# Performance work log

Measured on AMD Instinct MI355X. Metric: run time of the kernel, lower is better.

## Reference

```python
import jax, jax.numpy as jnp
import numpy as np

SEQ_DIM = 256
PAIR_DIM = 128
N_HEADS = 8
HIDDEN = 32
B, L = 4, 512


def layer_norm(x, gamma, beta, eps=1e-5):
    mu = jnp.mean(x, axis=-1, keepdims=True)
    var = jnp.var(x, axis=-1, keepdims=True)
    return (x - mu) * jax.lax.rsqrt(var + eps) * gamma + beta


def setup_inputs() -> dict:
    key = jax.random.key(0)
    ks = jax.random.split(key, 12)
    d = N_HEADS * HIDDEN
    s = 0.02
    return {
        "seq": jax.random.normal(ks[0], (B, L, SEQ_DIM), jnp.float32),
        "pair": jax.random.normal(ks[1], (B, L, L, PAIR_DIM), jnp.float32),
        "ln_seq_g": jnp.ones((SEQ_DIM,), jnp.float32),
        "ln_seq_b": jnp.zeros((SEQ_DIM,), jnp.float32),
        "ln_pair_g": jnp.ones((PAIR_DIM,), jnp.float32),
        "ln_pair_b": jnp.zeros((PAIR_DIM,), jnp.float32),
        "W_b": jax.random.normal(ks[2], (PAIR_DIM, N_HEADS), jnp.float32) * s,
        "W_q": jax.random.normal(ks[3], (SEQ_DIM, d), jnp.float32) * s,
        "W_k": jax.random.normal(ks[4], (SEQ_DIM, d), jnp.float32) * s,
        "W_v": jax.random.normal(ks[5], (SEQ_DIM, d), jnp.float32) * s,
        "W_g": jax.random.normal(ks[6], (SEQ_DIM, d), jnp.float32) * s,
        "b_g": jnp.zeros((d,), jnp.float32),
        "W_o": jax.random.normal(ks[7], (d, SEQ_DIM), jnp.float32) * s,
        "b_o": jnp.zeros((SEQ_DIM,), jnp.float32),
    }


def reference(seq, pair, ln_seq_g, ln_seq_b, ln_pair_g, ln_pair_b,
              W_b, W_q, W_k, W_v, W_g, b_g, W_o, b_o):
    b, l, _ = seq.shape
    factor = 1.0 / np.sqrt(HIDDEN).astype(np.float32)
    s = layer_norm(seq, ln_seq_g, ln_seq_b)
    p = layer_norm(pair, ln_pair_g, ln_pair_b)
    Q = (s @ W_q).reshape(b, l, N_HEADS, HIDDEN)
    K = (s @ W_k).reshape(b, l, N_HEADS, HIDDEN)
    V = (s @ W_v).reshape(b, l, N_HEADS, HIDDEN)
    # pair bias: [b, i, j, n] -> [b, n, i, j]
    bias = jnp.einsum('bijp,pn->bnij', p, W_b)
    att = jnp.einsum('binh,bjnh->bnij', Q, K) * factor + bias
    att = jax.nn.softmax(att, axis=-1)
    gate = jax.nn.sigmoid(s @ W_g + b_g).reshape(b, l, N_HEADS, HIDDEN)
    out = jnp.einsum('bnij,bjnh->binh', att, V) * gate
    out = out.reshape(b, l, N_HEADS * HIDDEN)
    return out @ W_o + b_o
```

## Files before the change

### kernel.cpp

```cpp
#include <hip/hip_runtime.h>
#include <math.h>

#define OFF_Q    0
#define OFF_K    (524288)
#define OFF_V    (524288*2)
#define OFF_G    (524288*3)
#define OFF_PRE  (524288*4)
#define OFF_BIAS (524288*5)

template <int CTRL>
__device__ __forceinline__ float dpp_mov(float x) {
  return __int_as_float(__builtin_amdgcn_update_dpp(0, __float_as_int(x), CTRL, 0xF, 0xF, true));
}
template <int CTRL>
__device__ __forceinline__ float dpp_add(float x) { return x + dpp_mov<CTRL>(x); }
__device__ __forceinline__ float red16(float v) {
  v = dpp_add<0xB1>(v);
  v = dpp_add<0x4E>(v);
  v = dpp_add<0x141>(v);
  v = dpp_add<0x140>(v);
  return v;
}

#define SEL8(a, f, out) do { \
  float _s0 = ((f)&1) ? a[1] : a[0]; \
  float _s1 = ((f)&1) ? a[3] : a[2]; \
  float _s2 = ((f)&1) ? a[5] : a[4]; \
  float _s3 = ((f)&1) ? a[7] : a[6]; \
  float _t0 = ((f)&2) ? _s1 : _s0; \
  float _t1 = ((f)&2) ? _s3 : _s2; \
  out = ((f)&4) ? _t1 : _t0; \
} while(0)

__device__ __forceinline__ float4 sel8_f4(const float4* a, int f) {
  float4 s0 = (f&1) ? a[1] : a[0];
  float4 s1 = (f&1) ? a[3] : a[2];
  float4 s2 = (f&1) ? a[5] : a[4];
  float4 s3 = (f&1) ? a[7] : a[6];
  float4 t0 = (f&2) ? s1 : s0;
  float4 t1 = (f&2) ? s3 : s2;
  return (f&4) ? t1 : t0;
}

__device__ __forceinline__ float dot4(float4 a, float4 b, float acc) {
  acc = fmaf(a.x, b.x, acc); acc = fmaf(a.y, b.y, acc);
  acc = fmaf(a.z, b.z, acc); return fmaf(a.w, b.w, acc);
}

template <int CTRL>
__device__ __forceinline__ void merge_dpp(float& m, float& l, float4* acc) {
  float m2 = dpp_mov<CTRL>(m);
  float l2 = dpp_mov<CTRL>(l);
  float M = fmaxf(m, m2);
  float ea = __expf(m - M), eb = __expf(m2 - M);
  l = l*ea + l2*eb;
#pragma unroll
  for (int x = 0; x < 8; ++x) {
    acc[x].x = acc[x].x*ea + dpp_mov<CTRL>(acc[x].x)*eb;
    acc[x].y = acc[x].y*ea + dpp_mov<CTRL>(acc[x].y)*eb;
    acc[x].z = acc[x].z*ea + dpp_mov<CTRL>(acc[x].z)*eb;
    acc[x].w = acc[x].w*ea + dpp_mov<CTRL>(acc[x].w)*eb;
  }
  m = M;
}

__global__ __launch_bounds__(256, 3) void k_mega(
    const float* __restrict__ seq, const float* __restrict__ lsg, const float* __restrict__ lsb,
    const float* __restrict__ lpg, const float* __restrict__ lpb, const float* __restrict__ Wb,
    const float* __restrict__ Wq, const float* __restrict__ Wk, const float* __restrict__ Wv,
    const float* __restrict__ Wg, const float* __restrict__ bg, const float* __restrict__ pair,
    float* __restrict__ Qw, float* __restrict__ Kw, float* __restrict__ Vw, float* __restrict__ Gw,
    float* __restrict__ biasw) {
  __shared__ __align__(16) float As[256*36];
  int t = threadIdx.x;
  int blk = blockIdx.x;

  if (blk >= 512) {
    int kb = blk - 512;
    int m0 = (kb >> 3) * 32;
    int y = kb & 7;
    {
      int r = t >> 3, c0 = t & 7;
      const float* srow = seq + (size_t)(m0 + r) * 256;
      float4 v[8];
      float s = 0.f, sq = 0.f;
#pragma unroll
      for (int qq = 0; qq < 8; ++qq) {
        v[qq] = *(const float4*)(srow + 4*(c0 + 8*qq));
        s += v[qq].x + v[qq].y + v[qq].z + v[qq].w;
        sq = fmaf(v[qq].x, v[qq].x, sq); sq = fmaf(v[qq].y, v[qq].y, sq);
        sq = fmaf(v[qq].z, v[qq].z, sq); sq = fmaf(v[qq].w, v[qq].w, sq);
      }
#pragma unroll
      for (int mm = 1; mm < 8; mm <<= 1) { s += __shfl_xor(s, mm); sq += __shfl_xor(sq, mm); }
      float mu = s * (1.f/256.f);
      float var = sq * (1.f/256.f) - mu*mu;
      float rstd = rsqrtf(var + 1e-5f);
#pragma unroll
      for (int qq = 0; qq < 8; ++qq) {
        int c4 = c0 + 8*qq;
        float4 g  = *(const float4*)(lsg + 4*c4);
        float4 bb = *(const float4*)(lsb + 4*c4);
        float* dp = As + 4*c4*36 + r;
        dp[0]   = (v[qq].x - mu)*rstd*g.x + bb.x;
        dp[36]  = (v[qq].y - mu)*rstd*g.y + bb.y;
        dp[72]  = (v[qq].z - mu)*rstd*g.z + bb.z;
        dp[108] = (v[qq].w - mu)*rstd*g.w + bb.w;
      }
    }
    __syncthreads();
    const float* Wm = (y < 2) ? Wq : (y < 4) ? Wk : (y < 6) ? Wv : Wg;
    int cb = (y & 1) * 128;
    int rg = t >> 5, cg2 = t & 31;
    const float* bp = Wm + cb + 4*cg2;
    const float* ap = As + 4*rg;
    float4 a0 = {0,0,0,0}, a1 = {0,0,0,0}, a2 = {0,0,0,0}, a3 = {0,0,0,0};
#pragma unroll 4
    for (int p = 0; p < 256; ++p) {
      float4 a  = *(const float4*)(ap + p*36);
      float4 bv = *(const float4*)(bp + p*256);
      a0.x = fmaf(a.x, bv.x, a0.x); a0.y = fmaf(a.x, bv.y, a0.y);
      a0.z = fmaf(a.x, bv.z, a0.z); a0.w = fmaf(a.x, bv.w, a0.w);
      a1.x = fmaf(a.y, bv.x, a1.x); a1.y = fmaf(a.y, bv.y, a1.y);
      a1.z = fmaf(a.y, bv.z, a1.z); a1.w = fmaf(a.y, bv.w, a1.w);
      a2.x = fmaf(a.z, bv.x, a2.x); a2.y = fmaf(a.z, bv.y, a2.y);
      a2.z = fmaf(a.z, bv.z, a2.z); a2.w = fmaf(a.z, bv.w, a2.w);
      a3.x = fmaf(a.w, bv.x, a3.x); a3.y = fmaf(a.w, bv.y, a3.y);
      a3.z = fmaf(a.w, bv.z, a3.z); a3.w = fmaf(a.w, bv.w, a3.w);
    }
    int mat = y >> 1;
    int col = cb + 4*cg2;
    float* outp = (mat == 0) ? Qw : (mat == 1) ? Kw : (mat == 2) ? Vw : Gw;
    if (mat == 0) {
      const float qs = 0.17677669529663687f;
      a0.x*=qs; a0.y*=qs; a0.z*=qs; a0.w*=qs;
      a1.x*=qs; a1.y*=qs; a1.z*=qs; a1.w*=qs;
      a2.x*=qs; a2.y*=qs; a2.z*=qs; a2.w*=qs;
      a3.x*=qs; a3.y*=qs; a3.z*=qs; a3.w*=qs;
    }
    if (mat == 3) {
      float4 g4 = *(const float4*)(bg + col);
      a0.x = 1.f/(1.f+__expf(-(a0.x+g4.x))); a0.y = 1.f/(1.f+__expf(-(a0.y+g4.y)));
      a0.z = 1.f/(1.f+__expf(-(a0.z+g4.z))); a0.w = 1.f/(1.f+__expf(-(a0.w+g4.w)));
      a1.x = 1.f/(1.f+__expf(-(a1.x+g4.x))); a1.y = 1.f/(1.f+__expf(-(a1.y+g4.y)));
      a1.z = 1.f/(1.f+__expf(-(a1.z+g4.z))); a1.w = 1.f/(1.f+__expf(-(a1.w+g4.w)));
      a2.x = 1.f/(1.f+__expf(-(a2.x+g4.x))); a2.y = 1.f/(1.f+__expf(-(a2.y+g4.y)));
      a2.z = 1.f/(1.f+__expf(-(a2.z+g4.z))); a2.w = 1.f/(1.f+__expf(-(a2.w+g4.w)));
      a3.x = 1.f/(1.f+__expf(-(a3.x+g4.x))); a3.y = 1.f/(1.f+__expf(-(a3.y+g4.y)));
      a3.z = 1.f/(1.f+__expf(-(a3.z+g4.z))); a3.w = 1.f/(1.f+__expf(-(a3.w+g4.w)));
    }
    int orow = m0 + 4*rg;
    *(float4*)(outp + (size_t)(orow+0)*256 + col) = a0;
    *(float4*)(outp + (size_t)(orow+1)*256 + col) = a1;
    *(float4*)(outp + (size_t)(orow+2)*256 + col) = a2;
    *(float4*)(outp + (size_t)(orow+3)*256 + col) = a3;
    return;
  }

  int lane = t & 63, w = t >> 6;
  int grp = lane >> 4, f = lane & 15;

  float wp[64];
  float cg[8] = {0,0,0,0,0,0,0,0}, cbv[8] = {0,0,0,0,0,0,0,0};
#pragma unroll
  for (int q = 0; q < 4; ++q) {
    int kA = 4*f + q, kB = 64 + 4*f + q;
    float gA = lpg[kA], bA = lpb[kA];
    float gB = lpg[kB], bB = lpb[kB];
    float4 uA0 = *(const float4*)(Wb + kA*8);
    float4 uA1 = *(const float4*)(Wb + kA*8 + 4);
    float4 uB0 = *(const float4*)(Wb + kB*8);
    float4 uB1 = *(const float4*)(Wb + kB*8 + 4);
    wp[q*8+0] = gA*uA0.x; cg[0] += wp[q*8+0]; cbv[0] = fmaf(bA, uA0.x, cbv[0]);
    wp[q*8+1] = gA*uA0.y; cg[1] += wp[q*8+1]; cbv[1] = fmaf(bA, uA0.y, cbv[1]);
    wp[q*8+2] = gA*uA0.z; cg[2] += wp[q*8+2]; cbv[2] = fmaf(bA, uA0.z, cbv[2]);
    wp[q*8+3] = gA*uA0.w; cg[3] += wp[q*8+3]; cbv[3] = fmaf(bA, uA0.w, cbv[3]);
    wp[q*8+4] = gA*uA1.x; cg[4] += wp[q*8+4]; cbv[4] = fmaf(bA, uA1.x, cbv[4]);
    wp[q*8+5] = gA*uA1.y; cg[5] += wp[q*8+5]; cbv[5] = fmaf(bA, uA1.y, cbv[5]);
    wp[q*8+6] = gA*uA1.z; cg[6] += wp[q*8+6]; cbv[6] = fmaf(bA, uA1.z, cbv[6]);
    wp[q*8+7] = gA*uA1.w; cg[7] += wp[q*8+7]; cbv[7] = fmaf(bA, uA1.w, cbv[7]);
    int qb8 = (4+q)*8;
    wp[qb8+0] = gB*uB0.x; cg[0] += wp[qb8+0]; cbv[0] = fmaf(bB, uB0.x, cbv[0]);
    wp[qb8+1] = gB*uB0.y; cg[1] += wp[qb8+1]; cbv[1] = fmaf(bB, uB0.y, cbv[1]);
    wp[qb8+2] = gB*uB0.z; cg[2] += wp[qb8+2]; cbv[2] = fmaf(bB, uB0.z, cbv[2]);
    wp[qb8+3] = gB*uB0.w; cg[3] += wp[qb8+3]; cbv[3] = fmaf(bB, uB0.w, cbv[3]);
    wp[qb8+4] = gB*uB1.x; cg[4] += wp[qb8+4]; cbv[4] = fmaf(bB, uB1.x, cbv[4]);
    wp[qb8+5] = gB*uB1.y; cg[5] += wp[qb8+5]; cbv[5] = fmaf(bB, uB1.y, cbv[5]);
    wp[qb8+6] = gB*uB1.z; cg[6] += wp[qb8+6]; cbv[6] = fmaf(bB, uB1.z, cbv[6]);
    wp[qb8+7] = gB*uB1.w; cg[7] += wp[qb8+7]; cbv[7] = fmaf(bB, uB1.w, cbv[7]);
  }
#pragma unroll
  for (int n2 = 0; n2 < 8; ++n2) { cg[n2] = red16(cg[n2]); cbv[n2] = red16(cbv[n2]); }
  float cgsel, cbsel;
  SEL8(cg, f, cgsel);
  SEL8(cbv, f, cbsel);

  int gid = blk*16 + w*4 + grp;
  const float* rp0 = pair + (size_t)gid*128 + 4*f;
  float* bw0 = biasw + (size_t)gid*8 + f;

#define PROCROW(X0, X1, IDX) { \
    float s_  = X0.x + X0.y + X0.z + X0.w + X1.x + X1.y + X1.z + X1.w; \
    float sq_ = X0.x*X0.x; \
    sq_ = fmaf(X0.y, X0.y, sq_); sq_ = fmaf(X0.z, X0.z, sq_); sq_ = fmaf(X0.w, X0.w, sq_); \
    sq_ = fmaf(X1.x, X1.x, sq_); sq_ = fmaf(X1.y, X1.y, sq_); \
    sq_ = fmaf(X1.z, X1.z, sq_); sq_ = fmaf(X1.w, X1.w, sq_); \
    float dd_[8]; \
    _Pragma("unroll") \
    for (int n2 = 0; n2 < 8; ++n2) { \
      float d_ = X0.x * wp[n2]; \
      d_ = fmaf(X0.y, wp[8+n2],  d_); \
      d_ = fmaf(X0.z, wp[16+n2], d_); \
      d_ = fmaf(X0.w, wp[24+n2], d_); \
      d_ = fmaf(X1.x, wp[32+n2], d_); \
      d_ = fmaf(X1.y, wp[40+n2], d_); \
      d_ = fmaf(X1.z, wp[48+n2], d_); \
      d_ = fmaf(X1.w, wp[56+n2], d_); \
      dd_[n2] = d_; \
    } \
    s_  = red16(s_); \
    sq_ = red16(sq_); \
    _Pragma("unroll") \
    for (int n2 = 0; n2 < 8; ++n2) dd_[n2] = red16(dd_[n2]); \
    float mu_ = s_ * (1.f/128.f); \
    float var_ = fmaf(sq_, 1.f/128.f, -mu_*mu_); \
    float rstd_ = rsqrtf(var_ + 1e-5f); \
    if (f < 8) { \
      float dv_; \
      SEL8(dd_, f, dv_); \
      bw0[(size_t)(IDX)*65536] = fmaf(rstd_, fmaf(-mu_, cgsel, dv_), cbsel); \
    } \
  }

  float4 A0[4], A1[4], B0[4], B1[4];
#pragma unroll
  for (int q = 0; q < 4; ++q) {
    const float* r = rp0 + (size_t)q*1048576;
    A0[q] = *(const float4*)r; A1[q] = *(const float4*)(r + 64);
  }
#pragma unroll
  for (int q = 0; q < 4; ++q) {
    const float* r = rp0 + (size_t)(4+q)*1048576;
    B0[q] = *(const float4*)r; B1[q] = *(const float4*)(r + 64);
  }

#define CHUNK(C0, C1, cc) { \
    _Pragma("unroll") \
    for (int q = 0; q < 4; ++q) PROCROW(C0[q], C1[q], (4*(cc) + q)); \
    if ((cc) + 2 < 32) { \
      _Pragma("unroll") \
      for (int q = 0; q < 4; ++q) { \
        const float* r = rp0 + (size_t)(4*((cc)+2) + q)*1048576; \
        C0[q] = *(const float4*)r; C1[q] = *(const float4*)(r + 64); \
      } \
    } \
  }

  for (int c = 0; c < 32; c += 2) {
    CHUNK(A0, A1, c)
    CHUNK(B0, B1, c+1)
  }
#undef CHUNK
#undef PROCROW
}

__global__ __launch_bounds__(512) void k_attn5(
    const float* __restrict__ Qw, const float* __restrict__ Kw, const float* __restrict__ Vw,
    const float* __restrict__ Gw, const float* __restrict__ biasw, float* __restrict__ prew) {
  __shared__ __align__(16) float Kb[2][32*292];
  __shared__ __align__(16) float Vb[2][32*292];
  float* scr = &Kb[0][0];

  int t = threadIdx.x, lane = t & 63, w = t >> 6;
  int b = blockIdx.x >> 6, i0 = (blockIdx.x & 63) << 3;
  int n = lane >> 3, js = lane & 7;
  int ip = w & 3, jset = w >> 2;
  int ila = 2*ip, ilb = ila + 1;
  size_t qra = (size_t)(b*512 + i0 + ila);
  size_t qrb = qra + 1;
  int jl0 = jset*16 + js;

  float4 qa[8], qb[8];
  {
    const float* pa = Qw + qra*256 + n*32;
    const float* pb = Qw + qrb*256 + n*32;
#pragma unroll
    for (int x = 0; x < 8; ++x) { qa[x] = *(const float4*)(pa + 4*x); qb[x] = *(const float4*)(pb + 4*x); }
  }
  float4 acca[8], accb[8];
#pragma unroll
  for (int x = 0; x < 8; ++x) { acca[x] = make_float4(0,0,0,0); accb[x] = make_float4(0,0,0,0); }
  float ma = -1e30f, la = 0.f, mb2 = -1e30f, lb2 = 0.f;

  const float* Kg = Kw + (size_t)(b*512)*256;
  const float* Vg = Vw + (size_t)(b*512)*256;
  const float* Bpa = biasw + ((size_t)(b*512 + i0 + ila)*512 + jl0)*8 + n;
  const float* Bpb = Bpa + 512*8;

  float4 sk[4], sv[4];
  int woff = (lane >> 3)*36 + (lane & 7)*4;

#define SLOAD(tn) { \
    const float* ks_ = Kg + ((size_t)(tn)*32 + 4*w)*256 + 4*lane; \
    const float* vs_ = Vg + ((size_t)(tn)*32 + 4*w)*256 + 4*lane; \
    sk[0] = *(const float4*)(ks_);       sk[1] = *(const float4*)(ks_ + 256); \
    sk[2] = *(const float4*)(ks_ + 512); sk[3] = *(const float4*)(ks_ + 768); \
    sv[0] = *(const float4*)(vs_);       sv[1] = *(const float4*)(vs_ + 256); \
    sv[2] = *(const float4*)(vs_ + 512); sv[3] = *(const float4*)(vs_ + 768); \
  }
#define SWRITE(tn) { int bf_ = (tn) & 1; \
    float* kd_ = &Kb[bf_][(4*w)*292 + woff]; \
    *(float4*)(kd_)       = sk[0]; *(float4*)(kd_ + 292) = sk[1]; \
    *(float4*)(kd_ + 584) = sk[2]; *(float4*)(kd_ + 876) = sk[3]; \
    float* vd_ = &Vb[bf_][(4*w)*292 + woff]; \
    *(float4*)(vd_)       = sv[0]; *(float4*)(vd_ + 292) = sv[1]; \
    *(float4*)(vd_ + 584) = sv[2]; *(float4*)(vd_ + 876) = sv[3]; \
  }

  SLOAD(0);
  SWRITE(0);
  __syncthreads();

  for (int tt = 0; tt < 16; ++tt) {
    int cur = tt & 1;
    if (tt < 15) SLOAD(tt+1);

    const float* Kt = Kb[cur];
    const float* Vt = Vb[cur];
    float bba0 = Bpa[tt*256], bba1 = Bpa[tt*256 + 64];
    float bbb0 = Bpb[tt*256], bbb1 = Bpb[tt*256 + 64];

    float lga0, lga1, lgb0, lgb1;
    {
      const float* kp = Kt + jl0*292 + n*36;
      float da = 0.f, db = 0.f;
#pragma unroll
      for (int x = 0; x < 8; ++x) {
        float4 kk = *(const float4*)(kp + 4*x);
        da = dot4(qa[x], kk, da); db = dot4(qb[x], kk, db);
      }
      lga0 = da + bba0; lgb0 = db + bbb0;
    }
    {
      const float* kp = Kt + (jl0+8)*292 + n*36;
      float da = 0.f, db = 0.f;
#pragma unroll
      for (int x = 0; x < 8; ++x) {
        float4 kk = *(const float4*)(kp + 4*x);
        da = dot4(qa[x], kk, da); db = dot4(qb[x], kk, db);
      }
      lga1 = da + bba1; lgb1 = db + bbb1;
    }
    {
      float tm = fmaxf(lga0, lga1);
      if (tm > ma) {
        float sc = __expf(ma - tm);
        la *= sc;
#pragma unroll
        for (int x = 0; x < 8; ++x) {
          acca[x].x *= sc; acca[x].y *= sc; acca[x].z *= sc; acca[x].w *= sc;
        }
        ma = tm;
      }
    }
    {
      float tm = fmaxf(lgb0, lgb1);
      if (tm > mb2) {
        float sc = __expf(mb2 - tm);
        lb2 *= sc;
#pragma unroll
        for (int x = 0; x < 8; ++x) {
          accb[x].x *= sc; accb[x].y *= sc; accb[x].z *= sc; accb[x].w *= sc;
        }
        mb2 = tm;
      }
    }
    float pa0 = __expf(lga0 - ma), pa1 = __expf(lga1 - ma);
    float pb0 = __expf(lgb0 - mb2), pb1 = __expf(lgb1 - mb2);
    la += pa0 + pa1; lb2 += pb0 + pb1;
    {
      const float* vp = Vt + jl0*292 + n*36;
#pragma unroll
      for (int x = 0; x < 8; ++x) {
        float4 vv = *(const float4*)(vp + 4*x);
        acca[x].x = fmaf(pa0, vv.x, acca[x].x); acca[x].y = fmaf(pa0, vv.y, acca[x].y);
        acca[x].z = fmaf(pa0, vv.z, acca[x].z); acca[x].w = fmaf(pa0, vv.w, acca[x].w);
        accb[x].x = fmaf(pb0, vv.x, accb[x].x); accb[x].y = fmaf(pb0, vv.y, accb[x].y);
        accb[x].z = fmaf(pb0, vv.z, accb[x].z); accb[x].w = fmaf(pb0, vv.w, accb[x].w);
      }
    }
    {
      const float* vp = Vt + (jl0+8)*292 + n*36;
#pragma unroll
      for (int x = 0; x < 8; ++x) {
        float4 vv = *(const float4*)(vp + 4*x);
        acca[x].x = fmaf(pa1, vv.x, acca[x].x); acca[x].y = fmaf(pa1, vv.y, acca[x].y);
        acca[x].z = fmaf(pa1, vv.z, acca[x].z); acca[x].w = fmaf(pa1, vv.w, acca[x].w);
        accb[x].x = fmaf(pb1, vv.x, accb[x].x); accb[x].y = fmaf(pb1, vv.y, accb[x].y);
        accb[x].z = fmaf(pb1, vv.z, accb[x].z); accb[x].w = fmaf(pb1, vv.w, accb[x].w);
      }
    }

    if (tt < 15) SWRITE(tt+1);
    __syncthreads();
  }
#undef SLOAD
#undef SWRITE

  merge_dpp<0xB1>(ma, la, acca);   merge_dpp<0xB1>(mb2, lb2, accb);
  merge_dpp<0x4E>(ma, la, acca);   merge_dpp<0x4E>(mb2, lb2, accb);
  merge_dpp<0x141>(ma, la, acca);  merge_dpp<0x141>(mb2, lb2, accb);

  float4 fa = sel8_f4(acca, js);
  float4 fb = sel8_f4(accb, js);

  if (jset == 1) {
    int base = (ip*8 + n)*68;
    *(float4*)(scr + base + 4*js) = fa;
    *(float4*)(scr + base + 32 + 4*js) = fb;
    if (js == 0) { scr[base+64] = ma; scr[base+65] = la; scr[base+66] = mb2; scr[base+67] = lb2; }
  }
  __syncthreads();
  if (jset == 0) {
    int base = (ip*8 + n)*68;
    float4 a2 = *(const float4*)(scr + base + 4*js);
    float4 b2 = *(const float4*)(scr + base + 32 + 4*js);
    float m2a = scr[base+64], l2a = scr[base+65];
    float m2b = scr[base+66], l2b = scr[base+67];
    {
      float M = fmaxf(ma, m2a);
      float ea = __expf(ma - M), eb = __expf(m2a - M);
      float inv = 1.f / (la*ea + l2a*eb);
      float4 g4 = *(const float4*)(Gw + qra*256 + n*32 + 4*js);
      float4 r;
      r.x = (fa.x*ea + a2.x*eb) * inv * g4.x;
      r.y = (fa.y*ea + a2.y*eb) * inv * g4.y;
      r.z = (fa.z*ea + a2.z*eb) * inv * g4.z;
      r.w = (fa.w*ea + a2.w*eb) * inv * g4.w;
      *(float4*)(prew + qra*256 + n*32 + 4*js) = r;
    }
    {
      float M = fmaxf(mb2, m2b);
      float ea = __expf(mb2 - M), eb = __expf(m2b - M);
      float inv = 1.f / (lb2*ea + l2b*eb);
      float4 g4 = *(const float4*)(Gw + qrb*256 + n*32 + 4*js);
      float4 r;
      r.x = (fb.x*ea + b2.x*eb) * inv * g4.x;
      r.y = (fb.y*ea + b2.y*eb) * inv * g4.y;
      r.z = (fb.z*ea + b2.z*eb) * inv * g4.z;
      r.w = (fb.w*ea + b2.w*eb) * inv * g4.w;
      *(float4*)(prew + qrb*256 + n*32 + 4*js) = r;
    }
  }
}

__global__ __launch_bounds__(256) void k_out(
    const float* __restrict__ prew, const float* __restrict__ Wo, const float* __restrict__ bo,
    float* __restrict__ out) {
  __shared__ __align__(16) float As[256*36];
  int t = threadIdx.x;
  int m0 = blockIdx.x * 32;
  int y = blockIdx.y;
  {
    int r = t >> 3, c0 = t & 7;
    const float* srow = prew + (size_t)(m0 + r)*256;
#pragma unroll
    for (int qq = 0; qq < 8; ++qq) {
      int c4 = c0 + 8*qq;
      float4 v = *(const float4*)(srow + 4*c4);
      float* dp = As + 4*c4*36 + r;
      dp[0] = v.x; dp[36] = v.y; dp[72] = v.z; dp[108] = v.w;
    }
  }
  __syncthreads();
  int cb = y*128;
  int rg = t >> 5, cg2 = t & 31;
  int col = cb + 4*cg2;
  const float* bp = Wo + col;
  const float* ap = As + 4*rg;
  float4 a0 = {0,0,0,0}, a1 = {0,0,0,0}, a2 = {0,0,0,0}, a3 = {0,0,0,0};
#pragma unroll 4
  for (int p = 0; p < 256; ++p) {
    float4 a  = *(const float4*)(ap + p*36);
    float4 bv = *(const float4*)(bp + p*256);
    a0.x = fmaf(a.x, bv.x, a0.x); a0.y = fmaf(a.x, bv.y, a0.y);
    a0.z = fmaf(a.x, bv.z, a0.z); a0.w = fmaf(a.x, bv.w, a0.w);
    a1.x = fmaf(a.y, bv.x, a1.x); a1.y = fmaf(a.y, bv.y, a1.y);
    a1.z = fmaf(a.y, bv.z, a1.z); a1.w = fmaf(a.y, bv.w, a1.w);
    a2.x = fmaf(a.z, bv.x, a2.x); a2.y = fmaf(a.z, bv.y, a2.y);
    a2.z = fmaf(a.z, bv.z, a2.z); a2.w = fmaf(a.z, bv.w, a2.w);
    a3.x = fmaf(a.w, bv.x, a3.x); a3.y = fmaf(a.w, bv.y, a3.y);
    a3.z = fmaf(a.w, bv.z, a3.z); a3.w = fmaf(a.w, bv.w, a3.w);
  }
  float4 b4 = *(const float4*)(bo + col);
  a0.x += b4.x; a0.y += b4.y; a0.z += b4.z; a0.w += b4.w;
  a1.x += b4.x; a1.y += b4.y; a1.z += b4.z; a1.w += b4.w;
  a2.x += b4.x; a2.y += b4.y; a2.z += b4.z; a2.w += b4.w;
  a3.x += b4.x; a3.y += b4.y; a3.z += b4.z; a3.w += b4.w;
  int orow = m0 + 4*rg;
  *(float4*)(out + (size_t)(orow+0)*256 + col) = a0;
  *(float4*)(out + (size_t)(orow+1)*256 + col) = a1;
  *(float4*)(out + (size_t)(orow+2)*256 + col) = a2;
  *(float4*)(out + (size_t)(orow+3)*256 + col) = a3;
}

extern "C" void kernel_launch(void* const* d_in, const int* in_sizes, int n_in,
                              void* d_out, int out_size, void* d_ws, size_t ws_size,
                              hipStream_t stream) {
  const float* seq  = (const float*)d_in[0];
  const float* pair = (const float*)d_in[1];
  const float* lsg  = (const float*)d_in[2];
  const float* lsb  = (const float*)d_in[3];
  const float* lpg  = (const float*)d_in[4];
  const float* lpb  = (const float*)d_in[5];
  const float* Wb   = (const float*)d_in[6];
  const float* Wq   = (const float*)d_in[7];
  const float* Wk   = (const float*)d_in[8];
  const float* Wv   = (const float*)d_in[9];
  const float* Wg   = (const float*)d_in[10];
  const float* bg   = (const float*)d_in[11];
  const float* Wo   = (const float*)d_in[12];
  const float* bo   = (const float*)d_in[13];
  float* ws   = (float*)d_ws;
  float* Qw   = ws + OFF_Q;
  float* Kw   = ws + OFF_K;
  float* Vw   = ws + OFF_V;
  float* Gw   = ws + OFF_G;
  float* prew = ws + OFF_PRE;
  float* biasw= ws + OFF_BIAS;
  float* out  = (float*)d_out;

  hipLaunchKernelGGL(k_mega, dim3(1024), dim3(256), 0, stream,
                     seq, lsg, lsb, lpg, lpb, Wb, Wq, Wk, Wv, Wg, bg, pair,
                     Qw, Kw, Vw, Gw, biasw);
  hipLaunchKernelGGL(k_attn5, dim3(256), dim3(512), 0, stream,
                     Qw, Kw, Vw, Gw, biasw, prew);
  hipLaunchKernelGGL(k_out, dim3(64, 2), dim3(256), 0, stream,
                     prew, Wo, bo, out);
}
```

Baseline: 205.7 us.

## Split attention into smaller blocks with four query rows and 16-key tiles

The attention kernel now runs 512 blocks of 256 threads instead of 256 blocks of 512 threads. Each block handles 4 query rows, and its K/V shared-memory tiles shrink to 16 keys, so each block steps through 32 tiles instead of 16. Each thread now processes one key per tile rather than two. The goal is a larger grid and lower shared memory per block, so two blocks can share a CU and latency is hidden better. The costs are twice the K/V global reads across the grid, twice as many barriers, and less work per thread to hide latency.

```diff
diff --git a/kernel.cpp b/kernel.cpp
--- a/kernel.cpp
+++ b/kernel.cpp
@@ -264,21 +264,22 @@
 #undef PROCROW
 }
 
-__global__ __launch_bounds__(512) void k_attn5(
+__global__ __launch_bounds__(256, 2) void k_attn6(
     const float* __restrict__ Qw, const float* __restrict__ Kw, const float* __restrict__ Vw,
     const float* __restrict__ Gw, const float* __restrict__ biasw, float* __restrict__ prew) {
-  __shared__ __align__(16) float Kb[2][32*292];
-  __shared__ __align__(16) float Vb[2][32*292];
+  __shared__ __align__(16) float Kb[2][16*292];
+  __shared__ __align__(16) float Vb[2][16*292];
   float* scr = &Kb[0][0];
 
   int t = threadIdx.x, lane = t & 63, w = t >> 6;
-  int b = blockIdx.x >> 6, i0 = (blockIdx.x & 63) << 3;
+  int b = blockIdx.x >> 7;
+  int i0 = (blockIdx.x & 127) << 2;
   int n = lane >> 3, js = lane & 7;
-  int ip = w & 3, jset = w >> 2;
+  int ip = w & 1, jset = w >> 1;
   int ila = 2*ip, ilb = ila + 1;
   size_t qra = (size_t)(b*512 + i0 + ila);
   size_t qrb = qra + 1;
-  int jl0 = jset*16 + js;
+  int jl0 = jset*8 + js;
 
   float4 qa[8], qb[8];
   {
@@ -301,8 +302,8 @@
   int woff = (lane >> 3)*36 + (lane & 7)*4;
 
 #define SLOAD(tn) { \
-    const float* ks_ = Kg + ((size_t)(tn)*32 + 4*w)*256 + 4*lane; \
-    const float* vs_ = Vg + ((size_t)(tn)*32 + 4*w)*256 + 4*lane; \
+    const float* ks_ = Kg + ((size_t)(tn)*16 + 4*w)*256 + 4*lane; \
+    const float* vs_ = Vg + ((size_t)(tn)*16 + 4*w)*256 + 4*lane; \
     sk[0] = *(const float4*)(ks_);       sk[1] = *(const float4*)(ks_ + 256); \
     sk[2] = *(const float4*)(ks_ + 512); sk[3] = *(const float4*)(ks_ + 768); \
     sv[0] = *(const float4*)(vs_);       sv[1] = *(const float4*)(vs_ + 256); \
@@ -321,16 +322,16 @@
   SWRITE(0);
   __syncthreads();
 
-  for (int tt = 0; tt < 16; ++tt) {
+  for (int tt = 0; tt < 32; ++tt) {
     int cur = tt & 1;
-    if (tt < 15) SLOAD(tt+1);
+    if (tt < 31) SLOAD(tt+1);
 
     const float* Kt = Kb[cur];
     const float* Vt = Vb[cur];
-    float bba0 = Bpa[tt*256], bba1 = Bpa[tt*256 + 64];
-    float bbb0 = Bpb[tt*256], bbb1 = Bpb[tt*256 + 64];
-
-    float lga0, lga1, lgb0, lgb1;
+    float bba = Bpa[tt*128];
+    float bbb = Bpb[tt*128];
+
+    float lga, lgb;
     {
       const float* kp = Kt + jl0*292 + n*36;
       float da = 0.f, db = 0.f;
@@ -339,69 +340,41 @@
         float4 kk = *(const float4*)(kp + 4*x);
         da = dot4(qa[x], kk, da); db = dot4(qb[x], kk, db);
       }
-      lga0 = da + bba0; lgb0 = db + bbb0;
-    }
-    {
-      const float* kp = Kt + (jl0+8)*292 + n*36;
-      float da = 0.f, db = 0.f;
+      lga = da + bba; lgb = db + bbb;
+    }
+    if (lga > ma) {
+      float sc = __expf(ma - lga);
+      la *= sc;
 #pragma unroll
       for (int x = 0; x < 8; ++x) {
-        float4 kk = *(const float4*)(kp + 4*x);
-        da = dot4(qa[x], kk, da); db = dot4(qb[x], kk, db);
+        acca[x].x *= sc; acca[x].y *= sc; acca[x].z *= sc; acca[x].w *= sc;
       }
-      lga1 = da + bba1; lgb1 = db + bbb1;
-    }
-    {
-      float tm = fmaxf(lga0, lga1);
-      if (tm > ma) {
-        float sc = __expf(ma - tm);
-        la *= sc;
-#pragma unroll
-        for (int x = 0; x < 8; ++x) {
-          acca[x].x *= sc; acca[x].y *= sc; acca[x].z *= sc; acca[x].w *= sc;
-        }
-        ma = tm;
+      ma = lga;
+    }
+    if (lgb > mb2) {
+      float sc = __expf(mb2 - lgb);
+      lb2 *= sc;
+#pragma unroll
+      for (int x = 0; x < 8; ++x) {
+        accb[x].x *= sc; accb[x].y *= sc; accb[x].z *= sc; accb[x].w *= sc;
       }
-    }
-    {
-      float tm = fmaxf(lgb0, lgb1);
-      if (tm > mb2) {
-        float sc = __expf(mb2 - tm);
-        lb2 *= sc;
-#pragma unroll
-        for (int x = 0; x < 8; ++x) {
-          accb[x].x *= sc; accb[x].y *= sc; accb[x].z *= sc; accb[x].w *= sc;
-        }
-        mb2 = tm;
-      }
-    }
-    float pa0 = __expf(lga0 - ma), pa1 = __expf(lga1 - ma);
-    float pb0 = __expf(lgb0 - mb2), pb1 = __expf(lgb1 - mb2);
-    la += pa0 + pa1; lb2 += pb0 + pb1;
+      mb2 = lgb;
+    }
+    float pa_ = __expf(lga - ma), pb_ = __expf(lgb - mb2);
+    la += pa_; lb2 += pb_;
     {
       const float* vp = Vt + jl0*292 + n*36;
 #pragma unroll
       for (int x = 0; x < 8; ++x) {
         float4 vv = *(const float4*)(vp + 4*x);
-        acca[x].x = fmaf(pa0, vv.x, acca[x].x); acca[x].y = fmaf(pa0, vv.y, acca[x].y);
-        acca[x].z = fmaf(pa0, vv.z, acca[x].z); acca[x].w = fmaf(pa0, vv.w, acca[x].w);
-        accb[x].x = fmaf(pb0, vv.x, accb[x].x); accb[x].y = fmaf(pb0, vv.y, accb[x].y);
-        accb[x].z = fmaf(pb0, vv.z, accb[x].z); accb[x].w = fmaf(pb0, vv.w, accb[x].w);
+        acca[x].x = fmaf(pa_, vv.x, acca[x].x); acca[x].y = fmaf(pa_, vv.y, acca[x].y);
+        acca[x].z = fmaf(pa_, vv.z, acca[x].z); acca[x].w = fmaf(pa_, vv.w, acca[x].w);
+        accb[x].x = fmaf(pb_, vv.x, accb[x].x); accb[x].y = fmaf(pb_, vv.y, accb[x].y);
+        accb[x].z = fmaf(pb_, vv.z, accb[x].z); accb[x].w = fmaf(pb_, vv.w, accb[x].w);
       }
     }
-    {
-      const float* vp = Vt + (jl0+8)*292 + n*36;
-#pragma unroll
-      for (int x = 0; x < 8; ++x) {
-        float4 vv = *(const float4*)(vp + 4*x);
-        acca[x].x = fmaf(pa1, vv.x, acca[x].x); acca[x].y = fmaf(pa1, vv.y, acca[x].y);
-        acca[x].z = fmaf(pa1, vv.z, acca[x].z); acca[x].w = fmaf(pa1, vv.w, acca[x].w);
-        accb[x].x = fmaf(pb1, vv.x, accb[x].x); accb[x].y = fmaf(pb1, vv.y, accb[x].y);
-        accb[x].z = fmaf(pb1, vv.z, accb[x].z); accb[x].w = fmaf(pb1, vv.w, accb[x].w);
-      }
-    }
-
-    if (tt < 15) SWRITE(tt+1);
+
+    if (tt < 31) SWRITE(tt+1);
     __syncthreads();
   }
 #undef SLOAD
@@ -533,7 +506,7 @@
   hipLaunchKernelGGL(k_mega, dim3(1024), dim3(256), 0, stream,
                      seq, lsg, lsb, lpg, lpb, Wb, Wq, Wk, Wv, Wg, bg, pair,
                      Qw, Kw, Vw, Gw, biasw);
-  hipLaunchKernelGGL(k_attn5, dim3(256), dim3(512), 0, stream,
+  hipLaunchKernelGGL(k_attn6, dim3(512), dim3(256), 0, stream,
                      Qw, Kw, Vw, Gw, biasw, prew);
   hipLaunchKernelGGL(k_out, dim3(64, 2), dim3(256), 0, stream,
                      prew, Wo, bo, out);
```

New measurement: 214.8 us. +4.4%, slower.
